# Optimization experiments

Hardware: AMD Instinct MI355X
Metric: run time of the kernel (lower is better)

The kernel has to match this reference:

```python
import jax, jax.numpy as jnp
import numpy as np
from functools import partial

N = 50000
IN_C, HID_C, OUT_C = 256, 128, 64
E = 800000


def gcn_norm(src, dst, n_nodes):
    # PyG gcn_norm with unit edge weights: deg from target index, D^-1/2 A D^-1/2
    ones = jnp.ones(src.shape[0], dtype=jnp.float32)
    deg = jax.ops.segment_sum(ones, dst, num_segments=n_nodes)
    dinv = jnp.where(deg > 0, jax.lax.rsqrt(deg), 0.0)
    return dinv[src] * dinv[dst]


def gcn_conv(x, src, dst, norm, W, b):
    h = x @ W                              # [N, out] dense GEMM first (PyG order)
    msg = h[src] * norm[:, None]           # gather + scale  [E', out]
    out = jax.ops.segment_sum(msg, dst, num_segments=x.shape[0])
    return out + b


def setup_inputs() -> dict:
    key = jax.random.key(0)
    ks = jax.random.split(key, 6)
    x = jax.random.normal(ks[0], (N, IN_C), dtype=jnp.float32)
    edge_index = jax.random.randint(ks[1], (2, E), 0, N, dtype=jnp.int32)
    # Glorot-ish init for weights
    W1 = jax.random.normal(ks[2], (IN_C, HID_C), dtype=jnp.float32) / np.sqrt(IN_C)
    b1 = jnp.zeros((HID_C,), dtype=jnp.float32)
    W2 = jax.random.normal(ks[3], (HID_C, OUT_C), dtype=jnp.float32) / np.sqrt(HID_C)
    b2 = jnp.zeros((OUT_C,), dtype=jnp.float32)
    return {"x": x, "edge_index": edge_index, "W1": W1, "b1": b1, "W2": W2, "b2": b2}


def reference(x, edge_index, W1, b1, W2, b2):
    # eval mode: dropout is identity
    n = x.shape[0]
    loop = jnp.arange(n, dtype=edge_index.dtype)
    src = jnp.concatenate([edge_index[0], loop])   # add self loops (static E+N)
    dst = jnp.concatenate([edge_index[1], loop])
    norm = gcn_norm(src, dst, n)
    h = jax.nn.relu(gcn_conv(x, src, dst, norm, W1, b1))
    return gcn_conv(h, src, dst, norm, W2, b2)
```

## Files before the change

### kernel.cpp

```cpp
#include <hip/hip_runtime.h>


#define TPB 256
#define NBKT 196
#define EB_CAP 4608
#define CSR_CAP 6400
#define P1_EPB 8192

typedef __bf16 bf16x8 __attribute__((ext_vector_type(8)));
typedef __bf16 bf16x4 __attribute__((ext_vector_type(4)));
typedef __bf16 bf16x2 __attribute__((ext_vector_type(2)));
typedef float f32x4 __attribute__((ext_vector_type(4)));

__device__ __forceinline__ float bflo(unsigned u) { return __uint_as_float(u << 16); }
__device__ __forceinline__ float bfhi(unsigned u) { return __uint_as_float(u & 0xffff0000u); }

__global__ __launch_bounds__(256) void clear_wprep_kernel(
    unsigned* __restrict__ gcnt, float* __restrict__ dinv, __bf16* __restrict__ h2s,
    int N,
    const float* __restrict__ W1, const float* __restrict__ W2,
    __bf16* __restrict__ wf1, __bf16* __restrict__ wf2) {
    if (blockIdx.x == 0) {
        int t = threadIdx.x;
        if (t < NBKT) gcnt[t] = 0;
        if (t == 0) dinv[N] = 0.0f;
        if (t < 32) ((unsigned*)(h2s + (long)N * 64))[t] = 0u;
        return;
    }
    int g = (blockIdx.x - 1) * TPB + threadIdx.x;
    if (g < 64 * 64) {
        int frag = g >> 6, L = g & 63;
        int kstep = frag >> 3, oct = frag & 7;
        int oc = oct * 16 + (L & 15);
        int k0 = kstep * 32 + (L >> 4) * 8;
        bf16x8 v;
#pragma unroll
        for (int j = 0; j < 8; j++) v[j] = (__bf16)W1[(k0 + j) * 128 + oc];
        ((bf16x8*)wf1)[g] = v;
    } else if (g < 64 * 64 + 16 * 64) {
        int g2 = g - 64 * 64;
        int frag = g2 >> 6, L = g2 & 63;
        int kstep = frag >> 2, oct = frag & 3;
        int oc = oct * 16 + (L & 15);
        int k0 = kstep * 32 + (L >> 4) * 8;
        bf16x8 v;
#pragma unroll
        for (int j = 0; j < 8; j++) v[j] = (__bf16)W2[(k0 + j) * 64 + oc];
        ((bf16x8*)wf2)[g2] = v;
    }
}

template <bool IN_BF16, int K, int OC, bool SCALE>
__device__ __forceinline__ void gemm_body(int bid, int tid, const void* __restrict__ Ain,
                                          const bf16x8* __restrict__ wfrag,
                                          const float* __restrict__ dinv,
                                          __bf16* __restrict__ outp, int M) {
    constexpr int KS = K / 32, OT = OC / 16;
    int wave = tid >> 6, lane = tid & 63;
    int col = lane & 15, q = lane >> 4;
    long rb = (long)bid * 128 + wave * 32;
    long r0 = rb + col, r1 = rb + 16 + col;
    long r0c = (r0 < M) ? r0 : (M - 1);
    long r1c = (r1 < M) ? r1 : (M - 1);

    f32x4 acc[OT][2];
#pragma unroll
    for (int o = 0; o < OT; o++) {
        acc[o][0] = (f32x4){0.f, 0.f, 0.f, 0.f};
        acc[o][1] = (f32x4){0.f, 0.f, 0.f, 0.f};
    }

#pragma unroll
    for (int ks = 0; ks < KS; ks++) {
        int k0 = ks * 32 + q * 8;
        bf16x8 b0, b1;
        if constexpr (IN_BF16) {
            const __bf16* A = (const __bf16*)Ain;
            b0 = *(const bf16x8*)(A + r0c * K + k0);
            b1 = *(const bf16x8*)(A + r1c * K + k0);
        } else {
            const float* A = (const float*)Ain;
            float4 f0a = *(const float4*)(A + r0c * K + k0);
            float4 f0b = *(const float4*)(A + r0c * K + k0 + 4);
            float4 f1a = *(const float4*)(A + r1c * K + k0);
            float4 f1b = *(const float4*)(A + r1c * K + k0 + 4);
            b0[0] = (__bf16)f0a.x; b0[1] = (__bf16)f0a.y; b0[2] = (__bf16)f0a.z; b0[3] = (__bf16)f0a.w;
            b0[4] = (__bf16)f0b.x; b0[5] = (__bf16)f0b.y; b0[6] = (__bf16)f0b.z; b0[7] = (__bf16)f0b.w;
            b1[0] = (__bf16)f1a.x; b1[1] = (__bf16)f1a.y; b1[2] = (__bf16)f1a.z; b1[3] = (__bf16)f1a.w;
            b1[4] = (__bf16)f1b.x; b1[5] = (__bf16)f1b.y; b1[6] = (__bf16)f1b.z; b1[7] = (__bf16)f1b.w;
        }
#pragma unroll
        for (int ot = 0; ot < OT; ot++) {
            bf16x8 a = wfrag[(ks * OT + ot) * 64 + lane];
            acc[ot][0] = __builtin_amdgcn_mfma_f32_16x16x32_bf16(a, b0, acc[ot][0], 0, 0, 0);
            acc[ot][1] = __builtin_amdgcn_mfma_f32_16x16x32_bf16(a, b1, acc[ot][1], 0, 0, 0);
        }
    }

    float sc0 = 1.f, sc1 = 1.f;
    if constexpr (SCALE) {
        sc0 = dinv[r0c];
        sc1 = dinv[r1c];
    }
#pragma unroll
    for (int ot = 0; ot < OT; ot++) {
        int oc = ot * 16 + q * 4;
        if (r0 < M) {
            bf16x4 v;
#pragma unroll
            for (int r = 0; r < 4; r++) v[r] = (__bf16)(acc[ot][0][r] * sc0);
            *(bf16x4*)(outp + r0 * OC + oc) = v;
        }
        if (r1 < M) {
            bf16x4 v;
#pragma unroll
            for (int r = 0; r < 4; r++) v[r] = (__bf16)(acc[ot][1][r] * sc1);
            *(bf16x4*)(outp + r1 * OC + oc) = v;
        }
    }
}

__global__ __launch_bounds__(256) void p1_gemm1_kernel(
    const int* __restrict__ src, const int* __restrict__ dst, int E, int p1Blocks,
    unsigned* __restrict__ gcnt, unsigned* __restrict__ ebuf,
    const float* __restrict__ x, const bf16x8* __restrict__ wf1,
    __bf16* __restrict__ h1u, int M) {
    __shared__ unsigned sPacked[P1_EPB];
    __shared__ int sCnt[256];
    if ((int)blockIdx.x < p1Blocks) {
        int t = threadIdx.x;
        sCnt[t] = 0;
        __syncthreads();
        long e0 = (long)blockIdx.x * P1_EPB;
        int cnt = (int)(E - e0);
        if (cnt > P1_EPB) cnt = P1_EPB;
        for (int i = t; i < cnt; i += 256) {
            unsigned s = (unsigned)src[e0 + i];
            unsigned d = (unsigned)dst[e0 + i];
            sPacked[i] = (s << 16) | d;
            atomicAdd(&sCnt[d >> 8], 1);
        }
        __syncthreads();
        int base = 0;
        if (t < NBKT) base = (int)atomicAdd(&gcnt[t], (unsigned)sCnt[t]);
        __syncthreads();
        if (t < NBKT) sCnt[t] = t * EB_CAP + base;
        __syncthreads();
        for (int i = t; i < cnt; i += 256) {
            unsigned p = sPacked[i];
            int b = (int)((p & 0xffffu) >> 8);
            int pos = atomicAdd(&sCnt[b], 1);
            if (pos < (b + 1) * EB_CAP) ebuf[pos] = p;
        }
    } else {
        gemm_body<false, 256, 128, false>(blockIdx.x - p1Blocks, threadIdx.x,
                                          x, wf1, nullptr, h1u, M);
    }
}

__global__ __launch_bounds__(256) void csr_kernel(
    const unsigned* __restrict__ gcnt, const unsigned* __restrict__ ebuf,
    int* __restrict__ csr, int2* __restrict__ se, float* __restrict__ dinv, int N) {
    __shared__ unsigned sEdges[EB_CAP];
    __shared__ int sCnt[256];
    __shared__ int sScan[256];
    int b = blockIdx.x, t = threadIdx.x;
    int m = (int)gcnt[b];
    if (m > EB_CAP) m = EB_CAP;
    sCnt[t] = 0;
    __syncthreads();
    const unsigned* eb = ebuf + b * EB_CAP;
    for (int i = t; i < m; i += 256) {
        unsigned p = eb[i];
        sEdges[i] = p;
        atomicAdd(&sCnt[p & 255u], 1);
    }
    __syncthreads();
    int c = sCnt[t];
    int pad = (c + 7) & ~7;
    sScan[t] = pad;
    __syncthreads();
    for (int off = 1; off < 256; off <<= 1) {
        int v = (t >= off) ? sScan[t - off] : 0;
        __syncthreads();
        sScan[t] += v;
        __syncthreads();
    }
    int start = b * CSR_CAP + sScan[t] - pad;
    int node = (b << 8) + t;
    if (node < N) {
        se[node] = make_int2(start, start + pad);
        dinv[node] = rsqrtf((float)c + 1.0f);
    }
    __syncthreads();
    sCnt[t] = start;
    __syncthreads();
    for (int i = t; i < m; i += 256) {
        unsigned p = sEdges[i];
        int pos = atomicAdd(&sCnt[p & 255u], 1);
        csr[pos] = (int)(p >> 16);
    }
    if (node < N) {
        for (int k = start + c; k < start + pad; k++) csr[k] = N;
    }
}

__global__ __launch_bounds__(256) void agg128_kernel(const __bf16* __restrict__ h,
                                                     const int* __restrict__ csr,
                                                     const int2* __restrict__ se,
                                                     const float* __restrict__ dinv,
                                                     const float* __restrict__ bias,
                                                     __bf16* __restrict__ outp, int N) {
    int gid = blockIdx.x * TPB + threadIdx.x;
    int n = gid >> 6, lane = gid & 63;
    if (n >= N) return;
    int2 s_e = se[n];
    int start = s_e.x, m = s_e.y - s_e.x;
    float dn = dinv[n];
    const unsigned* hp = (const unsigned*)h;
    const int* sl = csr + start;
    unsigned self = hp[(long)n * 64 + lane];
    float a0x = bflo(self) * dn, a0y = bfhi(self) * dn;
    float a1x = 0.f, a1y = 0.f, a2x = 0.f, a2y = 0.f, a3x = 0.f, a3y = 0.f;
    for (int j = 0; j < m; j += 8) {
        int4 e0 = *(const int4*)(sl + j);
        int4 e1 = *(const int4*)(sl + j + 4);
        unsigned v0 = hp[(long)e0.x * 64 + lane], v1 = hp[(long)e0.y * 64 + lane];
        unsigned v2 = hp[(long)e0.z * 64 + lane], v3 = hp[(long)e0.w * 64 + lane];
        unsigned v4 = hp[(long)e1.x * 64 + lane], v5 = hp[(long)e1.y * 64 + lane];
        unsigned v6 = hp[(long)e1.z * 64 + lane], v7 = hp[(long)e1.w * 64 + lane];
        float w0 = dinv[e0.x], w1 = dinv[e0.y], w2 = dinv[e0.z], w3 = dinv[e0.w];
        float w4 = dinv[e1.x], w5 = dinv[e1.y], w6 = dinv[e1.z], w7 = dinv[e1.w];
        a0x += bflo(v0) * w0; a0y += bfhi(v0) * w0;
        a1x += bflo(v1) * w1; a1y += bfhi(v1) * w1;
        a2x += bflo(v2) * w2; a2y += bfhi(v2) * w2;
        a3x += bflo(v3) * w3; a3y += bfhi(v3) * w3;
        a0x += bflo(v4) * w4; a0y += bfhi(v4) * w4;
        a1x += bflo(v5) * w5; a1y += bfhi(v5) * w5;
        a2x += bflo(v6) * w6; a2y += bfhi(v6) * w6;
        a3x += bflo(v7) * w7; a3y += bfhi(v7) * w7;
    }
    float2 bv = ((const float2*)bias)[lane];
    float ox = (a0x + a1x + a2x + a3x) * dn + bv.x;
    float oy = (a0y + a1y + a2y + a3y) * dn + bv.y;
    ox = fmaxf(ox, 0.f);
    oy = fmaxf(oy, 0.f);
    bf16x2 st = {(__bf16)ox, (__bf16)oy};
    ((bf16x2*)outp)[(long)n * 64 + lane] = st;
}

__global__ __launch_bounds__(256) void mfma_gemm2_kernel(const __bf16* __restrict__ Ain,
                                                         const bf16x8* __restrict__ wfrag,
                                                         const float* __restrict__ dinv,
                                                         __bf16* __restrict__ outp, int M) {
    gemm_body<true, 128, 64, true>(blockIdx.x, threadIdx.x, Ain, wfrag, dinv, outp, M);
}

__global__ __launch_bounds__(256) void agg64_kernel(const __bf16* __restrict__ hs,
                                                    const int* __restrict__ csr,
                                                    const int2* __restrict__ se,
                                                    const float* __restrict__ dinv,
                                                    const float* __restrict__ bias,
                                                    float* __restrict__ outp, int N) {
    int gid = blockIdx.x * TPB + threadIdx.x;
    int n = gid >> 6, lane = gid & 63;
    if (n >= N) return;
    int2 s_e = se[n];
    int start = s_e.x, m = s_e.y - s_e.x;
    float dn = dinv[n];
    const unsigned short* hp = (const unsigned short*)hs;
    const int* sl = csr + start;
    float a0 = __uint_as_float(((unsigned)hp[(long)n * 64 + lane]) << 16);
    float a1 = 0.f, a2 = 0.f, a3 = 0.f;
    for (int j = 0; j < m; j += 8) {
        int4 e0 = *(const int4*)(sl + j);
        int4 e1 = *(const int4*)(sl + j + 4);
        unsigned short v0 = hp[(long)e0.x * 64 + lane], v1 = hp[(long)e0.y * 64 + lane];
        unsigned short v2 = hp[(long)e0.z * 64 + lane], v3 = hp[(long)e0.w * 64 + lane];
        unsigned short v4 = hp[(long)e1.x * 64 + lane], v5 = hp[(long)e1.y * 64 + lane];
        unsigned short v6 = hp[(long)e1.z * 64 + lane], v7 = hp[(long)e1.w * 64 + lane];
        a0 += __uint_as_float((unsigned)v0 << 16); a1 += __uint_as_float((unsigned)v1 << 16);
        a2 += __uint_as_float((unsigned)v2 << 16); a3 += __uint_as_float((unsigned)v3 << 16);
        a0 += __uint_as_float((unsigned)v4 << 16); a1 += __uint_as_float((unsigned)v5 << 16);
        a2 += __uint_as_float((unsigned)v6 << 16); a3 += __uint_as_float((unsigned)v7 << 16);
    }
    outp[(long)n * 64 + lane] = (a0 + a1 + a2 + a3) * dn + bias[lane];
}

static inline int cdiv(long a, long b) { return (int)((a + b - 1) / b); }

extern "C" void kernel_launch(void* const* d_in, const int* in_sizes, int n_in,
                              void* d_out, int out_size, void* d_ws, size_t ws_size,
                              hipStream_t stream) {
    const float* x  = (const float*)d_in[0];
    const int*   ei = (const int*)d_in[1];
    const float* W1 = (const float*)d_in[2];
    const float* b1 = (const float*)d_in[3];
    const float* W2 = (const float*)d_in[4];
    const float* b2 = (const float*)d_in[5];

    const int IN_C = 256;
    const int N = in_sizes[0] / IN_C;
    const int E = in_sizes[1] / 2;
    const int* src = ei;
    const int* dst = ei + E;

    char* w = (char*)d_ws;
    size_t off = 0;
    auto alloc = [&](size_t bytes) { void* p = w + off; off = (off + bytes + 255) & ~255ull; return p; };
    __bf16*   h1u  = (__bf16*)alloc((size_t)(N + 1) * 128 * 2);
    __bf16*   agg1 = (__bf16*)alloc((size_t)N * 128 * 2);
    __bf16*   h2s  = (__bf16*)alloc((size_t)(N + 1) * 64 * 2);
    unsigned* ebuf = (unsigned*)alloc((size_t)NBKT * EB_CAP * 4);
    int*      csr  = (int*)alloc((size_t)NBKT * CSR_CAP * 4);
    int2*     se   = (int2*)alloc((size_t)N * 8);
    float*    dinv = (float*)alloc((size_t)(N + 1) * 4);
    unsigned* gcnt = (unsigned*)alloc(NBKT * 4);
    __bf16*   wf1  = (__bf16*)alloc(64 * 64 * 8 * 2);
    __bf16*   wf2  = (__bf16*)alloc(16 * 64 * 8 * 2);

    int wprepBlocks = cdiv(64 * 64 + 16 * 64, TPB);
    clear_wprep_kernel<<<1 + wprepBlocks, TPB, 0, stream>>>(gcnt, dinv, h2s, N,
                                                            W1, W2, wf1, wf2);

    int p1Blocks = cdiv(E, P1_EPB);
    int gemmBlocks = cdiv(N, 128);
    p1_gemm1_kernel<<<p1Blocks + gemmBlocks, TPB, 0, stream>>>(
        src, dst, E, p1Blocks, gcnt, ebuf, x, (const bf16x8*)wf1, h1u, N);

    csr_kernel<<<NBKT, TPB, 0, stream>>>(gcnt, ebuf, csr, se, dinv, N);

    agg128_kernel<<<cdiv((long)N * 64, TPB), TPB, 0, stream>>>(h1u, csr, se, dinv, b1, agg1, N);

    mfma_gemm2_kernel<<<gemmBlocks, TPB, 0, stream>>>(agg1, (const bf16x8*)wf2, dinv, h2s, N);

    agg64_kernel<<<cdiv((long)N * 64, TPB), TPB, 0, stream>>>(h2s, csr, se, dinv, b2,
                                                              (float*)d_out, N);
}
```

Measured before the change: 187.8 us.

## Widen per-lane gathers in aggregation kernels and drop LDS staging in bucketing

The aggregation kernels now have each lane load 8-byte chunks, so a wavefront processes two (128-ch) or four (64-ch) neighbor rows at once, with sub-groups combined via cross-lane shuffles at the end. The goal is fewer, wider gather instructions per edge and fewer loop iterations. The bucketing pass no longer stages packed edges in shared memory; it reads src/dst with int4 loads twice instead. This cuts LDS use, which may help occupancy for the co-scheduled GEMM blocks, at the cost of re-reading dst from global memory.

```diff
diff --git a/kernel.cpp b/kernel.cpp
--- a/kernel.cpp
+++ b/kernel.cpp
@@ -9,7 +9,6 @@
 
 typedef __bf16 bf16x8 __attribute__((ext_vector_type(8)));
 typedef __bf16 bf16x4 __attribute__((ext_vector_type(4)));
-typedef __bf16 bf16x2 __attribute__((ext_vector_type(2)));
 typedef float f32x4 __attribute__((ext_vector_type(4)));
 
 __device__ __forceinline__ float bflo(unsigned u) { return __uint_as_float(u << 16); }
@@ -125,7 +124,6 @@
     unsigned* __restrict__ gcnt, unsigned* __restrict__ ebuf,
     const float* __restrict__ x, const bf16x8* __restrict__ wf1,
     __bf16* __restrict__ h1u, int M) {
-    __shared__ unsigned sPacked[P1_EPB];
     __shared__ int sCnt[256];
     if ((int)blockIdx.x < p1Blocks) {
         int t = threadIdx.x;
@@ -134,11 +132,16 @@
         long e0 = (long)blockIdx.x * P1_EPB;
         int cnt = (int)(E - e0);
         if (cnt > P1_EPB) cnt = P1_EPB;
-        for (int i = t; i < cnt; i += 256) {
-            unsigned s = (unsigned)src[e0 + i];
-            unsigned d = (unsigned)dst[e0 + i];
-            sPacked[i] = (s << 16) | d;
-            atomicAdd(&sCnt[d >> 8], 1);
+        for (int i = t * 4; i < cnt; i += 1024) {
+            if (i + 4 <= cnt) {
+                int4 d = *(const int4*)(dst + e0 + i);
+                atomicAdd(&sCnt[d.x >> 8], 1);
+                atomicAdd(&sCnt[d.y >> 8], 1);
+                atomicAdd(&sCnt[d.z >> 8], 1);
+                atomicAdd(&sCnt[d.w >> 8], 1);
+            } else {
+                for (int k = i; k < cnt; k++) atomicAdd(&sCnt[dst[e0 + k] >> 8], 1);
+            }
         }
         __syncthreads();
         int base = 0;
@@ -146,11 +149,26 @@
         __syncthreads();
         if (t < NBKT) sCnt[t] = t * EB_CAP + base;
         __syncthreads();
-        for (int i = t; i < cnt; i += 256) {
-            unsigned p = sPacked[i];
-            int b = (int)((p & 0xffffu) >> 8);
-            int pos = atomicAdd(&sCnt[b], 1);
-            if (pos < (b + 1) * EB_CAP) ebuf[pos] = p;
+        for (int i = t * 4; i < cnt; i += 1024) {
+            if (i + 4 <= cnt) {
+                int4 d = *(const int4*)(dst + e0 + i);
+                int4 s = *(const int4*)(src + e0 + i);
+                int b0 = d.x >> 8, b1 = d.y >> 8, b2 = d.z >> 8, b3 = d.w >> 8;
+                int p0 = atomicAdd(&sCnt[b0], 1);
+                int p1 = atomicAdd(&sCnt[b1], 1);
+                int p2 = atomicAdd(&sCnt[b2], 1);
+                int p3 = atomicAdd(&sCnt[b3], 1);
+                if (p0 < (b0 + 1) * EB_CAP) ebuf[p0] = ((unsigned)s.x << 16) | (unsigned)d.x;
+                if (p1 < (b1 + 1) * EB_CAP) ebuf[p1] = ((unsigned)s.y << 16) | (unsigned)d.y;
+                if (p2 < (b2 + 1) * EB_CAP) ebuf[p2] = ((unsigned)s.z << 16) | (unsigned)d.z;
+                if (p3 < (b3 + 1) * EB_CAP) ebuf[p3] = ((unsigned)s.w << 16) | (unsigned)d.w;
+            } else {
+                for (int k = i; k < cnt; k++) {
+                    int dd = dst[e0 + k], b = dd >> 8;
+                    int p = atomicAdd(&sCnt[b], 1);
+                    if (p < (b + 1) * EB_CAP) ebuf[p] = ((unsigned)src[e0 + k] << 16) | (unsigned)dd;
+                }
+            }
         }
     } else {
         gemm_body<false, 256, 128, false>(blockIdx.x - p1Blocks, threadIdx.x,
@@ -214,39 +232,52 @@
     int gid = blockIdx.x * TPB + threadIdx.x;
     int n = gid >> 6, lane = gid & 63;
     if (n >= N) return;
+    int half = lane >> 5, l32 = lane & 31;
     int2 s_e = se[n];
     int start = s_e.x, m = s_e.y - s_e.x;
     float dn = dinv[n];
-    const unsigned* hp = (const unsigned*)h;
+    const uint2* hp = (const uint2*)h;
     const int* sl = csr + start;
-    unsigned self = hp[(long)n * 64 + lane];
-    float a0x = bflo(self) * dn, a0y = bfhi(self) * dn;
-    float a1x = 0.f, a1y = 0.f, a2x = 0.f, a2y = 0.f, a3x = 0.f, a3y = 0.f;
+    uint2 sv = hp[(long)n * 32 + l32];
+    float gate = (half == 0) ? dn : 0.f;
+    float a0 = bflo(sv.x) * gate, a1 = bfhi(sv.x) * gate;
+    float a2 = bflo(sv.y) * gate, a3 = bfhi(sv.y) * gate;
+    float c0 = 0.f, c1 = 0.f, c2 = 0.f, c3 = 0.f;
     for (int j = 0; j < m; j += 8) {
         int4 e0 = *(const int4*)(sl + j);
         int4 e1 = *(const int4*)(sl + j + 4);
-        unsigned v0 = hp[(long)e0.x * 64 + lane], v1 = hp[(long)e0.y * 64 + lane];
-        unsigned v2 = hp[(long)e0.z * 64 + lane], v3 = hp[(long)e0.w * 64 + lane];
-        unsigned v4 = hp[(long)e1.x * 64 + lane], v5 = hp[(long)e1.y * 64 + lane];
-        unsigned v6 = hp[(long)e1.z * 64 + lane], v7 = hp[(long)e1.w * 64 + lane];
-        float w0 = dinv[e0.x], w1 = dinv[e0.y], w2 = dinv[e0.z], w3 = dinv[e0.w];
-        float w4 = dinv[e1.x], w5 = dinv[e1.y], w6 = dinv[e1.z], w7 = dinv[e1.w];
-        a0x += bflo(v0) * w0; a0y += bfhi(v0) * w0;
-        a1x += bflo(v1) * w1; a1y += bfhi(v1) * w1;
-        a2x += bflo(v2) * w2; a2y += bfhi(v2) * w2;
-        a3x += bflo(v3) * w3; a3y += bfhi(v3) * w3;
-        a0x += bflo(v4) * w4; a0y += bfhi(v4) * w4;
-        a1x += bflo(v5) * w5; a1y += bfhi(v5) * w5;
-        a2x += bflo(v6) * w6; a2y += bfhi(v6) * w6;
-        a3x += bflo(v7) * w7; a3y += bfhi(v7) * w7;
-    }
-    float2 bv = ((const float2*)bias)[lane];
-    float ox = (a0x + a1x + a2x + a3x) * dn + bv.x;
-    float oy = (a0y + a1y + a2y + a3y) * dn + bv.y;
-    ox = fmaxf(ox, 0.f);
-    oy = fmaxf(oy, 0.f);
-    bf16x2 st = {(__bf16)ox, (__bf16)oy};
-    ((bf16x2*)outp)[(long)n * 64 + lane] = st;
+        int sA = half ? e0.y : e0.x;
+        int sB = half ? e0.w : e0.z;
+        int sC = half ? e1.y : e1.x;
+        int sD = half ? e1.w : e1.z;
+        uint2 vA = hp[(long)sA * 32 + l32];
+        uint2 vB = hp[(long)sB * 32 + l32];
+        uint2 vC = hp[(long)sC * 32 + l32];
+        uint2 vD = hp[(long)sD * 32 + l32];
+        float wA = dinv[sA], wB = dinv[sB], wC = dinv[sC], wD = dinv[sD];
+        a0 += bflo(vA.x) * wA; a1 += bfhi(vA.x) * wA;
+        a2 += bflo(vA.y) * wA; a3 += bfhi(vA.y) * wA;
+        c0 += bflo(vB.x) * wB; c1 += bfhi(vB.x) * wB;
+        c2 += bflo(vB.y) * wB; c3 += bfhi(vB.y) * wB;
+        a0 += bflo(vC.x) * wC; a1 += bfhi(vC.x) * wC;
+        a2 += bflo(vC.y) * wC; a3 += bfhi(vC.y) * wC;
+        c0 += bflo(vD.x) * wD; c1 += bfhi(vD.x) * wD;
+        c2 += bflo(vD.y) * wD; c3 += bfhi(vD.y) * wD;
+    }
+    a0 += c0; a1 += c1; a2 += c2; a3 += c3;
+    a0 += __shfl_xor(a0, 32, 64);
+    a1 += __shfl_xor(a1, 32, 64);
+    a2 += __shfl_xor(a2, 32, 64);
+    a3 += __shfl_xor(a3, 32, 64);
+    if (half == 0) {
+        float4 bv = ((const float4*)bias)[l32];
+        float o0 = fmaxf(a0 * dn + bv.x, 0.f);
+        float o1 = fmaxf(a1 * dn + bv.y, 0.f);
+        float o2 = fmaxf(a2 * dn + bv.z, 0.f);
+        float o3 = fmaxf(a3 * dn + bv.w, 0.f);
+        bf16x4 st = {(__bf16)o0, (__bf16)o1, (__bf16)o2, (__bf16)o3};
+        *(bf16x4*)(outp + (long)n * 128 + l32 * 4) = st;
+    }
 }
 
 __global__ __launch_bounds__(256) void mfma_gemm2_kernel(const __bf16* __restrict__ Ain,
@@ -265,26 +296,38 @@
     int gid = blockIdx.x * TPB + threadIdx.x;
     int n = gid >> 6, lane = gid & 63;
     if (n >= N) return;
+    int grp = lane >> 4, l16 = lane & 15;
     int2 s_e = se[n];
     int start = s_e.x, m = s_e.y - s_e.x;
     float dn = dinv[n];
-    const unsigned short* hp = (const unsigned short*)hs;
+    const uint2* hp = (const uint2*)hs;
     const int* sl = csr + start;
-    float a0 = __uint_as_float(((unsigned)hp[(long)n * 64 + lane]) << 16);
-    float a1 = 0.f, a2 = 0.f, a3 = 0.f;
+    uint2 sv = hp[(long)n * 16 + l16];
+    float gate = (grp == 0) ? 1.f : 0.f;
+    float a0 = bflo(sv.x) * gate, a1 = bfhi(sv.x) * gate;
+    float a2 = bflo(sv.y) * gate, a3 = bfhi(sv.y) * gate;
+    float c0 = 0.f, c1 = 0.f, c2 = 0.f, c3 = 0.f;
     for (int j = 0; j < m; j += 8) {
         int4 e0 = *(const int4*)(sl + j);
         int4 e1 = *(const int4*)(sl + j + 4);
-        unsigned short v0 = hp[(long)e0.x * 64 + lane], v1 = hp[(long)e0.y * 64 + lane];
-        unsigned short v2 = hp[(long)e0.z * 64 + lane], v3 = hp[(long)e0.w * 64 + lane];
-        unsigned short v4 = hp[(long)e1.x * 64 + lane], v5 = hp[(long)e1.y * 64 + lane];
-        unsigned short v6 = hp[(long)e1.z * 64 + lane], v7 = hp[(long)e1.w * 64 + lane];
-        a0 += __uint_as_float((unsigned)v0 << 16); a1 += __uint_as_float((unsigned)v1 << 16);
-        a2 += __uint_as_float((unsigned)v2 << 16); a3 += __uint_as_float((unsigned)v3 << 16);
-        a0 += __uint_as_float((unsigned)v4 << 16); a1 += __uint_as_float((unsigned)v5 << 16);
-        a2 += __uint_as_float((unsigned)v6 << 16); a3 += __uint_as_float((unsigned)v7 << 16);
-    }
-    outp[(long)n * 64 + lane] = (a0 + a1 + a2 + a3) * dn + bias[lane];
+        int sA = (grp & 2) ? ((grp & 1) ? e0.w : e0.z) : ((grp & 1) ? e0.y : e0.x);
+        int sB = (grp & 2) ? ((grp & 1) ? e1.w : e1.z) : ((grp & 1) ? e1.y : e1.x);
+        uint2 vA = hp[(long)sA * 16 + l16];
+        uint2 vB = hp[(long)sB * 16 + l16];
+        a0 += bflo(vA.x); a1 += bfhi(vA.x); a2 += bflo(vA.y); a3 += bfhi(vA.y);
+        c0 += bflo(vB.x); c1 += bfhi(vB.x); c2 += bflo(vB.y); c3 += bfhi(vB.y);
+    }
+    a0 += c0; a1 += c1; a2 += c2; a3 += c3;
+    a0 += __shfl_xor(a0, 16, 64); a0 += __shfl_xor(a0, 32, 64);
+    a1 += __shfl_xor(a1, 16, 64); a1 += __shfl_xor(a1, 32, 64);
+    a2 += __shfl_xor(a2, 16, 64); a2 += __shfl_xor(a2, 32, 64);
+    a3 += __shfl_xor(a3, 16, 64); a3 += __shfl_xor(a3, 32, 64);
+    if (lane < 16) {
+        float4 bv = ((const float4*)bias)[l16];
+        float4 o = make_float4(a0 * dn + bv.x, a1 * dn + bv.y,
+                               a2 * dn + bv.z, a3 * dn + bv.w);
+        *(float4*)(outp + (long)n * 64 + l16 * 4) = o;
+    }
 }
 
 static inline int cdiv(long a, long b) { return (int)((a + b - 1) / b); }
```

After: 200.2 us. 1.07x slower.
